# Kernel tuning notes

Hardware: AMD Instinct MI355X
Metric: run time of the kernel (lower is better)

## Reference

```python
import jax, jax.numpy as jnp
import numpy as np

V, D, C, L, F = 32000, 1024, 2048, 6, 4096
B, S = 2, 2048


def _layer_norm(x, w, b, eps=1e-5):
    mu = jnp.mean(x, axis=-1, keepdims=True)
    var = jnp.mean(jnp.square(x - mu), axis=-1, keepdims=True)
    return (x - mu) * jax.lax.rsqrt(var + eps) * w + b


def setup_inputs() -> dict:
    key = jax.random.key(0)
    ks = jax.random.split(key, 16)
    s = 0.02
    inp = {
        "tokens": jax.random.randint(ks[0], (B, S), 0, V),
        "embed_table": jax.random.normal(ks[1], (V, D), jnp.float32) * s,
        "pos_table": jax.random.normal(ks[2], (C, D), jnp.float32) * s,
        # stacked per-layer params [L, ...]
        "ln1_w": jnp.ones((L, D), jnp.float32),
        "ln1_b": jnp.zeros((L, D), jnp.float32),
        "qkv_w": jax.random.normal(ks[3], (L, 3 * D, D), jnp.float32) * s,
        "qkv_b": jnp.zeros((L, 3 * D), jnp.float32),
        "ln2_w": jnp.ones((L, D), jnp.float32),
        "ln2_b": jnp.zeros((L, D), jnp.float32),
        "ffa_w": jax.random.normal(ks[4], (L, F, D), jnp.float32) * s,
        "ffa_b": jnp.zeros((L, F), jnp.float32),
        "ffb_w": jax.random.normal(ks[5], (L, D, F), jnp.float32) * s,
        "ffb_b": jnp.zeros((L, D), jnp.float32),
        "out_w": jax.random.normal(ks[6], (V, D), jnp.float32) * s,
    }
    return inp


def _forward(tokens, embed_table, pos_table, ln1_w, ln1_b, qkv_w, qkv_b,
             ln2_w, ln2_b, ffa_w, ffa_b, ffb_w, ffb_b, out_w):
    Sx = tokens.shape[1]
    h = embed_table[tokens] + pos_table[:Sx][None, :, :]  # [B,S,D]
    causal = jnp.triu(jnp.ones((Sx, Sx), bool), k=1)       # True = masked
    scale = jnp.float32(D) ** 0.5

    def block(h, p):
        l1w, l1b, qw, qb, l2w, l2b, aw, ab, bw, bb = p
        a = _layer_norm(h, l1w, l1b)
        qkv = jnp.einsum('bsd,ed->bse', a, qw) + qb       # [B,S,3D]
        q, k, v = jnp.split(qkv, 3, axis=-1)
        scores = jnp.einsum('bsd,btd->bst', q, k)          # [B,S,S]
        scores = jnp.where(causal[None], -jnp.inf, scores)
        attn = jax.nn.softmax(scores / scale, axis=-1)
        h = h + jnp.einsum('bst,btd->bsd', attn, v)
        f = _layer_norm(h, l2w, l2b)
        f = jax.nn.relu(jnp.einsum('bsd,fd->bsf', f, aw) + ab)
        h = h + jnp.einsum('bsf,df->bsd', f, bw) + bb
        return h, None

    params = (ln1_w, ln1_b, qkv_w, qkv_b, ln2_w, ln2_b, ffa_w, ffa_b, ffb_w, ffb_b)
    h, _ = jax.lax.scan(block, h, params)
    # OutputLayer applies only the Linear (output_norm is defined but unused)
    return jnp.einsum('bsd,vd->bsv', h, out_w)


def reference(tokens, embed_table, pos_table, ln1_w, ln1_b, qkv_w, qkv_b,
              ln2_w, ln2_b, ffa_w, ffa_b, ffb_w, ffb_b, out_w):
    return _forward(tokens, embed_table, pos_table, ln1_w, ln1_b, qkv_w, qkv_b,
                    ln2_w, ln2_b, ffa_w, ffa_b, ffb_w, ffb_b, out_w)
```

## Files before the change

kernel.cpp:

```cpp
#include <hip/hip_runtime.h>

#define Dm 1024
#define Sm 2048
#define Bm 2
#define Lm 6
#define Fm 4096
#define Vm 32000
#define MT (Bm*Sm)

typedef unsigned short u16;
typedef unsigned int   u32;
typedef __attribute__((ext_vector_type(8))) short bf16x8;
typedef __attribute__((ext_vector_type(4))) float f32x4;

__device__ __forceinline__ u16 f2bf(float f) {
  u32 u = __float_as_uint(f);
  u += 0x7fffu + ((u >> 16) & 1u);
  return (u16)(u >> 16);
}
__device__ __forceinline__ u32 pack2(float a, float b) {
  return (u32)f2bf(a) | ((u32)f2bf(b) << 16);
}
__device__ __forceinline__ void gload16(const void* g, void* l) {
  __builtin_amdgcn_global_load_lds(
      (const __attribute__((address_space(1))) void*)g,
      (__attribute__((address_space(3))) void*)l, 16, 0, 0);
}

__global__ __launch_bounds__(256) void embed_kernel(
    const int* __restrict__ tok, const float* __restrict__ emb,
    const float* __restrict__ pos, float* __restrict__ h)
{
  int i  = blockIdx.x * 256 + threadIdx.x;
  int d  = (i & (Dm/4 - 1)) * 4;
  int bs = i >> 8;
  int s  = bs & (Sm - 1);
  int t  = tok[bs];
  float4 e = *(const float4*)(emb + (size_t)t * Dm + d);
  float4 p = *(const float4*)(pos + (size_t)s * Dm + d);
  float4 r; r.x = e.x + p.x; r.y = e.y + p.y; r.z = e.z + p.z; r.w = e.w + p.w;
  *(float4*)(h + (size_t)bs * Dm + d) = r;
}

__global__ __launch_bounds__(256) void ln_kernel(
    const float* __restrict__ x, const float* __restrict__ w,
    const float* __restrict__ b, u16* __restrict__ o)
{
  __shared__ float red[8];
  int row = blockIdx.x, tid = threadIdx.x;
  const float* xr = x + (size_t)row * Dm;
  float4 v = *(const float4*)(xr + tid * 4);
  float s1 = v.x + v.y + v.z + v.w;
  float s2 = v.x*v.x + v.y*v.y + v.z*v.z + v.w*v.w;
  #pragma unroll
  for (int off = 32; off; off >>= 1) {
    s1 += __shfl_down(s1, off, 64);
    s2 += __shfl_down(s2, off, 64);
  }
  int lane = tid & 63, wv = tid >> 6;
  if (!lane) { red[wv] = s1; red[4 + wv] = s2; }
  __syncthreads();
  s1 = red[0] + red[1] + red[2] + red[3];
  s2 = red[4] + red[5] + red[6] + red[7];
  float mu = s1 * (1.f / Dm);
  float rs = rsqrtf(s2 * (1.f / Dm) - mu * mu + 1e-5f);
  float4 wv4 = *(const float4*)(w + tid * 4);
  float4 bv4 = *(const float4*)(b + tid * 4);
  uint2 pk;
  pk.x = pack2((v.x - mu) * rs * wv4.x + bv4.x, (v.y - mu) * rs * wv4.y + bv4.y);
  pk.y = pack2((v.z - mu) * rs * wv4.z + bv4.z, (v.w - mu) * rs * wv4.w + bv4.w);
  *(uint2*)(o + (size_t)row * Dm + tid * 4) = pk;
}

__global__ __launch_bounds__(256) void softmax_kernel(
    const float* __restrict__ sc, u16* __restrict__ at)
{
  __shared__ float red[8];
  int gr = blockIdx.x;
  int s  = gr & (Sm - 1);
  const float* x = sc + (size_t)gr * Sm;
  u16* o = at + (size_t)gr * Sm;
  int tid = threadIdx.x;
  float4 v0 = *(const float4*)(x + tid * 8);
  float4 v1 = *(const float4*)(x + tid * 8 + 4);
  float vals[8] = {v0.x, v0.y, v0.z, v0.w, v1.x, v1.y, v1.z, v1.w};
  float mx = -1e30f;
  #pragma unroll
  for (int j = 0; j < 8; ++j) {
    int t = tid * 8 + j;
    vals[j] = (t <= s) ? vals[j] * 0.03125f : -1e30f;
    mx = fmaxf(mx, vals[j]);
  }
  #pragma unroll
  for (int off = 32; off; off >>= 1) mx = fmaxf(mx, __shfl_down(mx, off, 64));
  int lane = tid & 63, wv = tid >> 6;
  if (!lane) red[wv] = mx;
  __syncthreads();
  mx = fmaxf(fmaxf(red[0], red[1]), fmaxf(red[2], red[3]));
  __syncthreads();
  float e[8], sm = 0.f;
  #pragma unroll
  for (int j = 0; j < 8; ++j) {
    int t = tid * 8 + j;
    e[j] = (t <= s) ? __expf(vals[j] - mx) : 0.f;
    sm += e[j];
  }
  #pragma unroll
  for (int off = 32; off; off >>= 1) sm += __shfl_down(sm, off, 64);
  if (!lane) red[wv] = sm;
  __syncthreads();
  sm = red[0] + red[1] + red[2] + red[3];
  float inv = 1.f / sm;
  uint4 p;
  p.x = pack2(e[0]*inv, e[1]*inv); p.y = pack2(e[2]*inv, e[3]*inv);
  p.z = pack2(e[4]*inv, e[5]*inv); p.w = pack2(e[6]*inv, e[7]*inv);
  *(uint4*)(o + tid * 8) = p;
}

__global__ __launch_bounds__(256) void cvt8_kernel(
    const float* __restrict__ x, u16* __restrict__ o)
{
  size_t i = ((size_t)blockIdx.x * 256 + threadIdx.x) * 8;
  float4 v0 = *(const float4*)(x + i);
  float4 v1 = *(const float4*)(x + i + 4);
  uint4 p; p.x = pack2(v0.x, v0.y); p.y = pack2(v0.z, v0.w);
  p.z = pack2(v1.x, v1.y); p.w = pack2(v1.z, v1.w);
  *(uint4*)(o + i) = p;
}

__global__ __launch_bounds__(256) void cvtw_kernel(
    const float* __restrict__ qw, const float* __restrict__ aw,
    const float* __restrict__ bw, u16* __restrict__ o)
{
  int b = blockIdx.x;
  const float* src; u16* dst; int idx;
  if (b < 1536)      { src = qw; dst = o;                     idx = b; }
  else if (b < 3584) { src = aw; dst = o + 3*Dm*Dm;           idx = b - 1536; }
  else               { src = bw; dst = o + 3*Dm*Dm + Fm*Dm;   idx = b - 3584; }
  size_t i = ((size_t)idx * 256 + threadIdx.x) * 8;
  float4 v0 = *(const float4*)(src + i);
  float4 v1 = *(const float4*)(src + i + 4);
  uint4 p; p.x = pack2(v0.x, v0.y); p.y = pack2(v0.z, v0.w);
  p.z = pack2(v1.x, v1.y); p.w = pack2(v1.z, v1.w);
  *(uint4*)(dst + i) = p;
}

__global__ __launch_bounds__(256) void vtr_kernel(
    const u16* __restrict__ v, u16* __restrict__ vT)
{
  __shared__ u16 t[64][64];
  int b = blockIdx.z;
  int s0 = blockIdx.x * 64, d0 = blockIdx.y * 64;
  const u16* src = v + ((size_t)b * Sm + s0) * (3 * Dm) + d0;
  int tid = threadIdx.x;
  int rr = tid >> 3, cc = (tid & 7) * 8;
  #pragma unroll
  for (int it = 0; it < 2; ++it) {
    int r = rr + it * 32;
    uint4 x = *(const uint4*)(src + (size_t)r * (3 * Dm) + cc);
    *(uint4*)&t[r][cc ^ (((r >> 3) & 7) << 3)] = x;
  }
  __syncthreads();
  u16* dst = vT + ((size_t)b * Dm + d0) * Sm + s0;
  #pragma unroll
  for (int it = 0; it < 2; ++it) {
    int d = rr + it * 32;
    u16 tmp[8];
    #pragma unroll
    for (int j = 0; j < 8; ++j) {
      int r = cc + j;
      tmp[j] = t[r][d ^ (((r >> 3) & 7) << 3)];
    }
    *(uint4*)(dst + (size_t)d * Sm + cc) = *(uint4*)tmp;
  }
}

enum { EPI_F32 = 0, EPI_BF16 = 1, EPI_RELU_BF16 = 2, EPI_RES = 3, EPI_F32NT = 4 };

__global__ __launch_bounds__(256, 2)
void gemm_kernel(const u16* __restrict__ A, const u16* __restrict__ B,
                 float* __restrict__ outF, u16* __restrict__ outB,
                 const float* __restrict__ bias, const float* __restrict__ resid,
                 int N, int K, int lda, int ldb,
                 long sA, long sB, long sO, long sR,
                 int mshift, int epi, int swz)
{
  __shared__ __align__(16) short As[128 * 64];
  __shared__ __align__(16) short Bs[128 * 64];

  const int z = blockIdx.z;
  int bid = blockIdx.x;
  if (swz) { int cpx = gridDim.x >> 3; bid = (bid & 7) * cpx + (bid >> 3); }
  const int m0 = (bid & ((1 << mshift) - 1)) << 7;
  const int n0 = (bid >> mshift) << 7;

  const u16* Az = A + (size_t)z * sA;
  const u16* Bz = B + (size_t)z * sB;

  const int tid = threadIdx.x;
  const int l   = tid & 63;
  const int w   = tid >> 6;
  const int sub = l >> 3;
  const int colb = ((l & 7) ^ sub) << 4;
  const int row0 = w * 32 + sub;

  const char* gA = (const char*)(Az + (size_t)(m0 + row0) * lda) + colb;
  const char* gB = (const char*)(Bz + (size_t)(n0 + row0) * ldb) + colb;
  const size_t stepA = (size_t)8 * lda * 2;
  const size_t stepB = (size_t)8 * ldb * 2;
  char* lA = (char*)As + w * 4096;
  char* lB = (char*)Bs + w * 4096;

  const int wm   = (w >> 1) * 64;
  const int wn   = (w & 1) * 64;
  const int lrow = l & 15;
  const int kgrp = l >> 4;

  f32x4 acc[4][4];
  #pragma unroll
  for (int i = 0; i < 4; ++i)
    #pragma unroll
    for (int j = 0; j < 4; ++j)
      acc[i][j] = (f32x4){0.f, 0.f, 0.f, 0.f};

  for (int k0 = 0; k0 < K; k0 += 64) {
    __syncthreads();
    const char* ga = gA + (size_t)k0 * 2;
    const char* gb = gB + (size_t)k0 * 2;
    #pragma unroll
    for (int c = 0; c < 4; ++c) {
      gload16(ga + c * stepA, lA + c * 1024);
      gload16(gb + c * stepB, lB + c * 1024);
    }
    __syncthreads();
    #pragma unroll
    for (int kk = 0; kk < 2; ++kk) {
      bf16x8 af[4], bf_[4];
      #pragma unroll
      for (int i = 0; i < 4; ++i) {
        int ar = wm + i * 16 + lrow;
        af[i]  = *(const bf16x8*)((const char*)As + ar * 128 +
                                  ((kk * 64 + kgrp * 16) ^ ((ar & 7) << 4)));
        int br = wn + i * 16 + lrow;
        bf_[i] = *(const bf16x8*)((const char*)Bs + br * 128 +
                                  ((kk * 64 + kgrp * 16) ^ ((br & 7) << 4)));
      }
      #pragma unroll
      for (int i = 0; i < 4; ++i)
        #pragma unroll
        for (int j = 0; j < 4; ++j)
          acc[i][j] = __builtin_amdgcn_mfma_f32_16x16x32_bf16(af[i], bf_[j], acc[i][j], 0, 0, 0);
    }
  }

  #pragma unroll
  for (int i = 0; i < 4; ++i) {
    #pragma unroll
    for (int j = 0; j < 4; ++j) {
      #pragma unroll
      for (int r = 0; r < 4; ++r) {
        int m = m0 + wm + i * 16 + kgrp * 4 + r;
        int n = n0 + wn + j * 16 + lrow;
        float v = acc[i][j][r];
        if (bias) v += bias[n];
        if (epi == EPI_F32) {
          outF[(size_t)z * sO + (size_t)m * N + n] = v;
        } else if (epi == EPI_BF16) {
          outB[(size_t)m * N + n] = f2bf(v);
        } else if (epi == EPI_RELU_BF16) {
          outB[(size_t)m * N + n] = f2bf(fmaxf(v, 0.f));
        } else {
          float* o = outF + (size_t)z * sO;
          const float* rsd = resid + (size_t)z * sR;
          o[(size_t)m * N + n] = rsd[(size_t)m * N + n] + v;
        }
      }
    }
  }
}

#define BAR_IN()  { __builtin_amdgcn_s_barrier(); \
                    asm volatile("s_waitcnt lgkmcnt(0)" ::: "memory"); \
                    __builtin_amdgcn_sched_barrier(0); \
                    __builtin_amdgcn_s_setprio(1); }
#define BAR_OUT() { __builtin_amdgcn_s_setprio(0); \
                    __builtin_amdgcn_sched_barrier(0); \
                    __builtin_amdgcn_s_barrier(); }

__global__ __launch_bounds__(512, 2)
void gemm256_kernel(const u16* __restrict__ A, const u16* __restrict__ B,
                    float* __restrict__ outF, u16* __restrict__ outB,
                    const float* __restrict__ bias,
                    int N, int K, int mshift, int epi)
{
  extern __shared__ char lds[];

  int bid = blockIdx.x;
  { int cpx = gridDim.x >> 3; bid = (bid & 7) * cpx + (bid >> 3); }
  const int m0 = (bid & ((1 << mshift) - 1)) << 8;
  const int n0 = (bid >> mshift) << 8;

  const int tid = threadIdx.x;
  const int l = tid & 63, w = tid >> 6;
  const int wr = w >> 2, wc = w & 3;
  const int lrow = l & 15, kgrp = l >> 4;
  const int wrbase = wr * 128, wcbase = wc * 64;
  const int srow = (w << 3) + (l >> 3);
  const int scol = ((l & 7) ^ (l >> 3)) << 3;
  const int nt = K >> 6;

  f32x4 acc[8][4];
  #pragma unroll
  for (int i = 0; i < 8; ++i)
    #pragma unroll
    for (int j = 0; j < 4; ++j)
      acc[i][j] = (f32x4){0.f, 0.f, 0.f, 0.f};

  auto STG = [&](int slot, const u16* gb, int grow0, int kel) {
    const u16* g = gb + (size_t)(grow0 + srow) * K + kel + scol;
    gload16(g, lds + slot + w * 1024);
    gload16(g + (size_t)64 * K, lds + slot + 8192 + w * 1024);
  };

  STG(0,              A, m0,       0);
  STG(16384,          A, m0 + 128, 0);
  STG(32768,          B, n0,       0);
  STG(49152,          B, n0 + 128, 0);
  STG(65536 + 32768,  B, n0,       64);
  STG(65536 + 49152,  B, n0 + 128, 64);
  asm volatile("s_waitcnt vmcnt(4)" ::: "memory");
  __builtin_amdgcn_s_barrier();

  bf16x8 af[4][2], bfr[4][2];

  #define RDA(base, q) { _Pragma("unroll") \
    for (int f2 = 0; f2 < 4; ++f2) { _Pragma("unroll") \
      for (int kk = 0; kk < 2; ++kk) { \
        int row = wrbase + (q) * 64 + f2 * 16 + lrow; \
        af[f2][kk] = *(const bf16x8*)((base) + row * 128 + \
                       ((kk * 64 + kgrp * 16) ^ ((row & 7) << 4))); } } }
  #define RDB(base, h) { _Pragma("unroll") \
    for (int j2 = 0; j2 < 2; ++j2) { _Pragma("unroll") \
      for (int kk = 0; kk < 2; ++kk) { \
        int row = wcbase + ((h) * 2 + j2) * 16 + lrow; \
        bfr[(h) * 2 + j2][kk] = *(const bf16x8*)((base) + row * 128 + \
                       ((kk * 64 + kgrp * 16) ^ ((row & 7) << 4))); } } }
  #define MM(fi0, fj0) { _Pragma("unroll") \
    for (int f2 = 0; f2 < 4; ++f2) { _Pragma("unroll") \
      for (int j2 = 0; j2 < 2; ++j2) { _Pragma("unroll") \
        for (int kk = 0; kk < 2; ++kk) \
          acc[(fi0) + f2][(fj0) + j2] = __builtin_amdgcn_mfma_f32_16x16x32_bf16( \
              af[f2][kk], bfr[(fj0) + j2][kk], acc[(fi0) + f2][(fj0) + j2], 0, 0, 0); } } }

  for (int i = 0; i < (nt >> 1); ++i) {
    const int ta = 2 * i, tb = 2 * i + 1;
    const int kA  = tb << 6;
    const int kN0 = (ta + 2 < nt ? ta + 2 : ta + 2 - nt) << 6;
    const int kN1 = (tb + 2 < nt ? tb + 2 : tb + 2 - nt) << 6;
    const char* cA = lds;
    const char* cB = lds + 32768;
    RDA(cA, 0); RDB(cB, 0);
    STG(65536, A, m0, kA);
    BAR_IN(); MM(0, 0); BAR_OUT();
    RDB(cB, 1);
    STG(65536 + 16384, A, m0 + 128, kA);
    BAR_IN(); MM(0, 2); BAR_OUT();
    RDA(cA, 1);
    STG(32768, B, n0, kN0);
    BAR_IN(); MM(4, 0); BAR_OUT();
    STG(49152, B, n0 + 128, kN0);
    BAR_IN(); MM(4, 2);
    __builtin_amdgcn_s_setprio(0);
    __builtin_amdgcn_sched_barrier(0);
    asm volatile("s_waitcnt vmcnt(4)" ::: "memory");
    __builtin_amdgcn_s_barrier();
    cA = lds + 65536; cB = lds + 65536 + 32768;
    RDA(cA, 0); RDB(cB, 0);
    STG(0, A, m0, kN0);
    BAR_IN(); MM(0, 0); BAR_OUT();
    RDB(cB, 1);
    STG(16384, A, m0 + 128, kN0);
    BAR_IN(); MM(0, 2); BAR_OUT();
    RDA(cA, 1);
    STG(65536 + 32768, B, n0, kN1);
    BAR_IN(); MM(4, 0); BAR_OUT();
    STG(65536 + 49152, B, n0 + 128, kN1);
    BAR_IN(); MM(4, 2);
    __builtin_amdgcn_s_setprio(0);
    __builtin_amdgcn_sched_barrier(0);
    asm volatile("s_waitcnt vmcnt(4)" ::: "memory");
    __builtin_amdgcn_s_barrier();
  }

  #pragma unroll
  for (int fi = 0; fi < 8; ++fi) {
    #pragma unroll
    for (int fj = 0; fj < 4; ++fj) {
      #pragma unroll
      for (int r = 0; r < 4; ++r) {
        int m = m0 + wrbase + fi * 16 + kgrp * 4 + r;
        int n = n0 + wcbase + fj * 16 + lrow;
        float v = acc[fi][fj][r];
        if (bias) v += bias[n];
        if (epi == EPI_F32) {
          outF[(size_t)m * N + n] = v;
        } else if (epi == EPI_F32NT) {
          __builtin_nontemporal_store(v, outF + (size_t)m * N + n);
        } else if (epi == EPI_BF16) {
          outB[(size_t)m * N + n] = f2bf(v);
        } else {
          outB[(size_t)m * N + n] = f2bf(fmaxf(v, 0.f));
        }
      }
    }
  }
}

extern "C" void kernel_launch(void* const* d_in, const int* in_sizes, int n_in,
                              void* d_out, int out_size, void* d_ws, size_t ws_size,
                              hipStream_t stream)
{
  const int*   tok  = (const int*)d_in[0];
  const float* emb  = (const float*)d_in[1];
  const float* pos  = (const float*)d_in[2];
  const float* ln1w = (const float*)d_in[3];
  const float* ln1b = (const float*)d_in[4];
  const float* qkvw = (const float*)d_in[5];
  const float* qkvb = (const float*)d_in[6];
  const float* ln2w = (const float*)d_in[7];
  const float* ln2b = (const float*)d_in[8];
  const float* ffaw = (const float*)d_in[9];
  const float* ffab = (const float*)d_in[10];
  const float* ffbw = (const float*)d_in[11];
  const float* ffbb = (const float*)d_in[12];
  const float* outw = (const float*)d_in[13];
  float* out = (float*)d_out;

  static bool attr_set = false;
  hipFuncSetAttribute((const void*)gemm256_kernel,
                      hipFuncAttributeMaxDynamicSharedMemorySize, 131072);
  (void)attr_set;

  char* p = (char*)d_ws;
  float* h      = (float*)p;  p += (size_t)MT * Dm * 4;
  u16*   a      = (u16*)p;    p += (size_t)MT * Dm * 2;
  u16*   hb     = (u16*)p;    p += (size_t)MT * Dm * 2;
  u16*   qkv    = (u16*)p;    p += (size_t)MT * 3 * Dm * 2;
  u16*   vT     = (u16*)p;    p += (size_t)Bm * Dm * Sm * 2;
  float* scores = (float*)p;  p += (size_t)Bm * Sm * Sm * 4;
  u16*   attn   = (u16*)p;    p += (size_t)Bm * Sm * Sm * 2;
  u16*   f      = (u16*)p;    p += (size_t)MT * Fm * 2;
  u16*   wlb    = (u16*)p;    p += (size_t)(3*Dm*Dm + Fm*Dm + Dm*Fm) * 2;
  u16*   owb    = qkv;

  embed_kernel<<<MT * Dm / 1024, 256, 0, stream>>>(tok, emb, pos, h);

  for (int l = 0; l < Lm; ++l) {
    cvtw_kernel<<<5632, 256, 0, stream>>>(
        qkvw + (size_t)l * 3 * Dm * Dm, ffaw + (size_t)l * Fm * Dm,
        ffbw + (size_t)l * Dm * Fm, wlb);
    ln_kernel<<<MT, 256, 0, stream>>>(h, ln1w + l * Dm, ln1b + l * Dm, a);
    gemm256_kernel<<<dim3(192), 512, 131072, stream>>>(
        a, wlb, nullptr, qkv, qkvb + l * 3 * Dm, 3 * Dm, Dm, 4, EPI_BF16);
    gemm_kernel<<<dim3(256, 1, Bm), 256, 0, stream>>>(
        qkv, qkv + Dm, scores, nullptr, nullptr, nullptr,
        Sm, Dm, 3 * Dm, 3 * Dm, (long)Sm * 3 * Dm, (long)Sm * 3 * Dm,
        (long)Sm * Sm, 0, 4, EPI_F32, 0);
    softmax_kernel<<<Bm * Sm, 256, 0, stream>>>(scores, attn);
    vtr_kernel<<<dim3(32, 16, Bm), 256, 0, stream>>>(qkv + 2 * Dm, vT);
    gemm_kernel<<<dim3(128, 1, Bm), 256, 0, stream>>>(
        attn, vT, h, nullptr, nullptr, h,
        Dm, Sm, Sm, Sm, (long)Sm * Sm, (long)Dm * Sm,
        (long)Sm * Dm, (long)Sm * Dm, 4, EPI_RES, 0);
    ln_kernel<<<MT, 256, 0, stream>>>(h, ln2w + l * Dm, ln2b + l * Dm, a);
    gemm256_kernel<<<dim3(256), 512, 131072, stream>>>(
        a, wlb + 3 * Dm * Dm, nullptr, f, ffab + l * Fm, Fm, Dm, 4, EPI_RELU_BF16);
    gemm_kernel<<<dim3(256, 1, 1), 256, 0, stream>>>(
        f, wlb + 3 * Dm * Dm + Fm * Dm, h, nullptr, ffbb + l * Dm, h,
        Dm, Fm, Fm, Fm, 0, 0, 0, 0, 5, EPI_RES, 1);
  }

  cvt8_kernel<<<MT * Dm / 2048, 256, 0, stream>>>(h, hb);
  cvt8_kernel<<<Vm * Dm / 2048, 256, 0, stream>>>(outw, owb);
  gemm256_kernel<<<dim3(2000), 512, 131072, stream>>>(
      hb, owb, out, nullptr, nullptr, Vm, Dm, 4, EPI_F32NT);
}
```

Measured before the change: 2.301 ms.

## Skip causally masked tiles in attention GEMMs and drop wraparound prefetches

Adds a cmode parameter to the 128x128 GEMM. In mode 1 (QK^T) blocks entirely above the diagonal exit early. In mode 2 (attn·V) the K loop stops at the diagonal, so roughly half the attention matmul work is skipped. The 256-tile GEMM pipeline is also restructured: the last iteration is peeled so it no longer issues wraparound loads of already-used K tiles, and A-tile prefetches are rescheduled with adjusted vmcnt waits. This relies on the softmax producing zeros for masked positions without reading the now-unwritten upper score tiles as valid data.

```diff
diff --git a/kernel.cpp b/kernel.cpp
--- a/kernel.cpp
+++ b/kernel.cpp
@@ -183,7 +183,7 @@
                  const float* __restrict__ bias, const float* __restrict__ resid,
                  int N, int K, int lda, int ldb,
                  long sA, long sB, long sO, long sR,
-                 int mshift, int epi, int swz)
+                 int mshift, int epi, int swz, int cmode)
 {
   __shared__ __align__(16) short As[128 * 64];
   __shared__ __align__(16) short Bs[128 * 64];
@@ -193,6 +193,9 @@
   if (swz) { int cpx = gridDim.x >> 3; bid = (bid & 7) * cpx + (bid >> 3); }
   const int m0 = (bid & ((1 << mshift) - 1)) << 7;
   const int n0 = (bid >> mshift) << 7;
+
+  if (cmode == 1 && n0 > m0) return;
+  const int keff = (cmode == 2) ? min(K, m0 + 128) : K;
 
   const u16* Az = A + (size_t)z * sA;
   const u16* Bz = B + (size_t)z * sB;
@@ -223,7 +226,7 @@
     for (int j = 0; j < 4; ++j)
       acc[i][j] = (f32x4){0.f, 0.f, 0.f, 0.f};
 
-  for (int k0 = 0; k0 < K; k0 += 64) {
+  for (int k0 = 0; k0 < keff; k0 += 64) {
     __syncthreads();
     const char* ga = gA + (size_t)k0 * 2;
     const char* gb = gB + (size_t)k0 * 2;
@@ -328,7 +331,8 @@
   STG(49152,          B, n0 + 128, 0);
   STG(65536 + 32768,  B, n0,       64);
   STG(65536 + 49152,  B, n0 + 128, 64);
-  asm volatile("s_waitcnt vmcnt(4)" ::: "memory");
+  STG(65536,          A, m0,       64);
+  asm volatile("s_waitcnt vmcnt(6)" ::: "memory");
   __builtin_amdgcn_s_barrier();
 
   bf16x8 af[4][2], bfr[4][2];
@@ -352,44 +356,68 @@
           acc[(fi0) + f2][(fj0) + j2] = __builtin_amdgcn_mfma_f32_16x16x32_bf16( \
               af[f2][kk], bfr[(fj0) + j2][kk], acc[(fi0) + f2][(fj0) + j2], 0, 0, 0); } } }
 
-  for (int i = 0; i < (nt >> 1); ++i) {
-    const int ta = 2 * i, tb = 2 * i + 1;
-    const int kA  = tb << 6;
-    const int kN0 = (ta + 2 < nt ? ta + 2 : ta + 2 - nt) << 6;
-    const int kN1 = (tb + 2 < nt ? tb + 2 : tb + 2 - nt) << 6;
-    const char* cA = lds;
-    const char* cB = lds + 32768;
-    RDA(cA, 0); RDB(cB, 0);
-    STG(65536, A, m0, kA);
+  const char* c0A = lds;
+  const char* c0B = lds + 32768;
+  const char* c1A = lds + 65536;
+  const char* c1B = lds + 65536 + 32768;
+
+  for (int i = 0; i < (nt >> 1) - 1; ++i) {
+    const int kA1 = (2 * i + 1) << 6;
+    const int kN0 = (2 * i + 2) << 6;
+    const int kN1 = (2 * i + 3) << 6;
+    RDA(c0A, 0); RDB(c0B, 0);
+    STG(65536 + 16384, A, m0 + 128, kA1);
     BAR_IN(); MM(0, 0); BAR_OUT();
-    RDB(cB, 1);
-    STG(65536 + 16384, A, m0 + 128, kA);
+    RDB(c0B, 1);
     BAR_IN(); MM(0, 2); BAR_OUT();
-    RDA(cA, 1);
+    RDA(c0A, 1);
     STG(32768, B, n0, kN0);
     BAR_IN(); MM(4, 0); BAR_OUT();
     STG(49152, B, n0 + 128, kN0);
+    STG(0,     A, m0,       kN0);
+    STG(16384, A, m0 + 128, kN0);
     BAR_IN(); MM(4, 2);
     __builtin_amdgcn_s_setprio(0);
     __builtin_amdgcn_sched_barrier(0);
-    asm volatile("s_waitcnt vmcnt(4)" ::: "memory");
+    asm volatile("s_waitcnt vmcnt(8)" ::: "memory");
     __builtin_amdgcn_s_barrier();
-    cA = lds + 65536; cB = lds + 65536 + 32768;
-    RDA(cA, 0); RDB(cB, 0);
-    STG(0, A, m0, kN0);
+    RDA(c1A, 0); RDB(c1B, 0);
     BAR_IN(); MM(0, 0); BAR_OUT();
-    RDB(cB, 1);
-    STG(16384, A, m0 + 128, kN0);
+    RDB(c1B, 1);
     BAR_IN(); MM(0, 2); BAR_OUT();
-    RDA(cA, 1);
+    RDA(c1A, 1);
     STG(65536 + 32768, B, n0, kN1);
     BAR_IN(); MM(4, 0); BAR_OUT();
     STG(65536 + 49152, B, n0 + 128, kN1);
+    STG(65536,         A, m0,       kN1);
     BAR_IN(); MM(4, 2);
     __builtin_amdgcn_s_setprio(0);
     __builtin_amdgcn_sched_barrier(0);
-    asm volatile("s_waitcnt vmcnt(4)" ::: "memory");
+    asm volatile("s_waitcnt vmcnt(6)" ::: "memory");
     __builtin_amdgcn_s_barrier();
+  }
+
+  {
+    RDA(c0A, 0); RDB(c0B, 0);
+    STG(65536 + 16384, A, m0 + 128, (nt - 1) << 6);
+    BAR_IN(); MM(0, 0); BAR_OUT();
+    RDB(c0B, 1);
+    BAR_IN(); MM(0, 2); BAR_OUT();
+    RDA(c0A, 1);
+    BAR_IN(); MM(4, 0); BAR_OUT();
+    BAR_IN(); MM(4, 2);
+    __builtin_amdgcn_s_setprio(0);
+    __builtin_amdgcn_sched_barrier(0);
+    asm volatile("s_waitcnt vmcnt(0)" ::: "memory");
+    __builtin_amdgcn_s_barrier();
+    RDA(c1A, 0); RDB(c1B, 0);
+    BAR_IN(); MM(0, 0); BAR_OUT();
+    RDB(c1B, 1);
+    BAR_IN(); MM(0, 2); BAR_OUT();
+    RDA(c1A, 1);
+    BAR_IN(); MM(4, 0); BAR_OUT();
+    BAR_IN(); MM(4, 2);
+    __builtin_amdgcn_s_setprio(0);
   }
 
   #pragma unroll
@@ -436,10 +464,8 @@
   const float* outw = (const float*)d_in[13];
   float* out = (float*)d_out;
 
-  static bool attr_set = false;
   hipFuncSetAttribute((const void*)gemm256_kernel,
                       hipFuncAttributeMaxDynamicSharedMemorySize, 131072);
-  (void)attr_set;
 
   char* p = (char*)d_ws;
   float* h      = (float*)p;  p += (size_t)MT * Dm * 4;
@@ -465,19 +491,19 @@
     gemm_kernel<<<dim3(256, 1, Bm), 256, 0, stream>>>(
         qkv, qkv + Dm, scores, nullptr, nullptr, nullptr,
         Sm, Dm, 3 * Dm, 3 * Dm, (long)Sm * 3 * Dm, (long)Sm * 3 * Dm,
-        (long)Sm * Sm, 0, 4, EPI_F32, 0);
+        (long)Sm * Sm, 0, 4, EPI_F32, 0, 1);
     softmax_kernel<<<Bm * Sm, 256, 0, stream>>>(scores, attn);
     vtr_kernel<<<dim3(32, 16, Bm), 256, 0, stream>>>(qkv + 2 * Dm, vT);
     gemm_kernel<<<dim3(128, 1, Bm), 256, 0, stream>>>(
         attn, vT, h, nullptr, nullptr, h,
         Dm, Sm, Sm, Sm, (long)Sm * Sm, (long)Dm * Sm,
-        (long)Sm * Dm, (long)Sm * Dm, 4, EPI_RES, 0);
+        (long)Sm * Dm, (long)Sm * Dm, 4, EPI_RES, 0, 2);
     ln_kernel<<<MT, 256, 0, stream>>>(h, ln2w + l * Dm, ln2b + l * Dm, a);
     gemm256_kernel<<<dim3(256), 512, 131072, stream>>>(
         a, wlb + 3 * Dm * Dm, nullptr, f, ffab + l * Fm, Fm, Dm, 4, EPI_RELU_BF16);
     gemm_kernel<<<dim3(256, 1, 1), 256, 0, stream>>>(
         f, wlb + 3 * Dm * Dm + Fm * Dm, h, nullptr, ffbb + l * Dm, h,
-        Dm, Fm, Fm, Fm, 0, 0, 0, 0, 5, EPI_RES, 1);
+        Dm, Fm, Fm, Fm, 0, 0, 0, 0, 5, EPI_RES, 1, 0);
   }
 
   cvt8_kernel<<<MT * Dm / 2048, 256, 0, stream>>>(h, hb);
```

New measurement: 2.338 ms. About the same (+1.6%).
